# Kernel optimization log

Hardware: AMD Instinct MI355X
Metric: run time of the kernel (lower is better)

Reference implementation:

```python
import jax, jax.numpy as jnp
import numpy as np

NUM_USERS = 60000
NUM_ITEMS = 40000
NUM_NODES = NUM_USERS + NUM_ITEMS
EMBED_DIM = 64
NUM_LAYERS = 3
NUM_EDGES = 1200000
BATCH = 16384


def setup_inputs() -> dict:
    key = jax.random.key(0)
    ks = jax.random.split(key, 7)
    user_indices = jax.random.randint(ks[0], (BATCH,), 0, NUM_USERS)
    item_indices = jax.random.randint(ks[1], (BATCH,), 0, NUM_ITEMS)
    edge_rows = jax.random.randint(ks[2], (NUM_EDGES,), 0, NUM_NODES)
    edge_cols = jax.random.randint(ks[3], (NUM_EDGES,), 0, NUM_NODES)
    # normalized adjacency values are small positives ~ 1/sqrt(deg_i*deg_j)
    edge_vals = jax.random.uniform(ks[4], (NUM_EDGES,), dtype=jnp.float32) * 0.1
    # xavier_uniform for Embedding(num, dim): bound = sqrt(6/(num+dim))
    bu = float(np.sqrt(6.0 / (NUM_USERS + EMBED_DIM)))
    bi = float(np.sqrt(6.0 / (NUM_ITEMS + EMBED_DIM)))
    user_emb = jax.random.uniform(ks[5], (NUM_USERS, EMBED_DIM), jnp.float32, -bu, bu)
    item_emb = jax.random.uniform(ks[6], (NUM_ITEMS, EMBED_DIM), jnp.float32, -bi, bi)
    return {
        "user_indices": user_indices,
        "item_indices": item_indices,
        "edge_rows": edge_rows,
        "edge_cols": edge_cols,
        "edge_vals": edge_vals,
        "user_emb": user_emb,
        "item_emb": item_emb,
    }


def _spmm(edge_rows, edge_cols, edge_vals, x):
    # out[i] = sum_{e: rows[e]==i} vals[e] * x[cols[e]]  -- COO SpMM
    msgs = edge_vals[:, None] * x[edge_cols]  # [E, D]
    return jax.ops.segment_sum(msgs, edge_rows, num_segments=NUM_NODES)


def reference(user_indices, item_indices, edge_rows, edge_cols, edge_vals,
              user_emb, item_emb):
    all_embeds = jnp.concatenate([user_emb, item_emb], axis=0)  # [N, D]
    for _ in range(NUM_LAYERS):
        all_embeds = _spmm(edge_rows, edge_cols, edge_vals, all_embeds)
    all_users = all_embeds[:NUM_USERS]
    all_items = all_embeds[NUM_USERS:]
    u = all_users[user_indices]  # [B, D]
    v = all_items[item_indices]  # [B, D]
    return jnp.sum(u * v, axis=1)  # [B]
```

## Files before the change

kernel.cpp:

```cpp
#include <hip/hip_runtime.h>

#define NUM_USERS 60000
#define NUM_ITEMS 40000
#define NUM_NODES 100000
#define DIM       64
#define NUM_EDGES 1200000
#define BATCH     16384

#define BROWS 256
#define NBUCK 391
#define CAP   4096
#define EPB   4096
#define BINBLK 512
#define ZWORDS (512 + 256 + 3200)

__device__ __forceinline__ unsigned short f2bf(float f) {
    unsigned u = __float_as_uint(f);
    unsigned r = (u + 0x7FFFu + ((u >> 16) & 1u)) >> 16;
    return (unsigned short)r;
}

__global__ __launch_bounds__(256) void convert_emb(
    const float4* __restrict__ ue, const float4* __restrict__ ie,
    ushort4* __restrict__ xc, int* __restrict__ zbase)
{
    if (blockIdx.x == 0)
        for (int i = threadIdx.x; i < ZWORDS; i += 256) zbase[i] = 0;
    const int nU4 = NUM_USERS * (DIM / 4);
    const int total4 = NUM_NODES * (DIM / 4);
    int i = blockIdx.x * blockDim.x + threadIdx.x;
    int stride = gridDim.x * blockDim.x;
    for (; i < total4; i += stride) {
        float4 v = (i < nU4) ? ue[i] : ie[i - nU4];
        ushort4 s;
        s.x = f2bf(v.x); s.y = f2bf(v.y); s.z = f2bf(v.z); s.w = f2bf(v.w);
        xc[i] = s;
    }
}

__global__ __launch_bounds__(BINBLK) void bin_edges(
    const int* __restrict__ rows, const int* __restrict__ cols,
    const float* __restrict__ vals,
    const int* __restrict__ uidx, const int* __restrict__ iidx,
    int* __restrict__ gcursor, unsigned* __restrict__ flags,
    unsigned long long* __restrict__ tmp)
{
    __shared__ int cnt[NBUCK], lcur[NBUCK], gbase[NBUCK];
    int t = threadIdx.x;
    for (int i = t; i < NBUCK; i += BINBLK) { cnt[i] = 0; lcur[i] = 0; }
    int fbase = blockIdx.x * 112;
    for (int k = t; k < 112; k += BINBLK) {
        int gi = fbase + k;
        if (gi < BATCH) {
            int n = uidx[gi];
            atomicOr(&flags[n >> 5], 1u << (n & 31));
        } else if (gi < 2 * BATCH) {
            int n = NUM_USERS + iidx[gi - BATCH];
            atomicOr(&flags[n >> 5], 1u << (n & 31));
        }
    }
    __syncthreads();
    int base = blockIdx.x * EPB;
    int lim = NUM_EDGES - base; if (lim > EPB) lim = EPB;
    for (int k = t; k < lim; k += BINBLK)
        atomicAdd(&cnt[rows[base + k] >> 8], 1);
    __syncthreads();
    for (int i = t; i < NBUCK; i += BINBLK) {
        int c = cnt[i];
        gbase[i] = c ? atomicAdd(&gcursor[i], c) : 0;
    }
    __syncthreads();
    for (int k = t; k < lim; k += BINBLK) {
        int idx = base + k;
        int r = rows[idx];
        int b = r >> 8;
        int lofs = atomicAdd(&lcur[b], 1);
        unsigned long long packed =
            ((unsigned long long)(unsigned)__float_as_int(vals[idx]) << 32)
            | ((unsigned)(r & 255) << 17) | (unsigned)cols[idx];
        tmp[(size_t)b * CAP + gbase[b] + lofs] = packed;
    }
}

__global__ __launch_bounds__(256) void sort_buckets(
    const unsigned long long* __restrict__ tmp, const int* __restrict__ gcursor,
    int2* __restrict__ rse, int2* __restrict__ csr)
{
    __shared__ int lcnt[BROWS], rowcur[BROWS], sdata[BROWS];
    __shared__ int2 stage[CAP];
    int b = blockIdx.x;
    int t = threadIdx.x;
    int count = gcursor[b];
    int base  = b * CAP;
    const unsigned long long* src = tmp + (size_t)base;
    lcnt[t] = 0;
    __syncthreads();
    for (int i = t; i < count; i += 256)
        atomicAdd(&lcnt[(int)((src[i] >> 17) & 255)], 1);
    __syncthreads();
    int myc = lcnt[t];
    sdata[t] = myc;
    __syncthreads();
    #pragma unroll
    for (int off = 1; off < 256; off <<= 1) {
        int x = (t >= off) ? sdata[t - off] : 0;
        __syncthreads();
        sdata[t] += x;
        __syncthreads();
    }
    int excl = sdata[t] - myc;
    rowcur[t] = excl;
    int row = b * BROWS + t;
    if (row < NUM_NODES)
        rse[row] = make_int2(base + excl, base + excl + myc);
    __syncthreads();
    for (int i = t; i < count; i += 256) {
        unsigned long long v = src[i];
        int lr = (int)((v >> 17) & 255);
        int pos = atomicAdd(&rowcur[lr], 1);
        stage[pos] = make_int2((int)(v & 0x1FFFF), (int)(v >> 32));
    }
    __syncthreads();
    for (int i = t; i < count; i += 256)
        csr[(size_t)base + i] = stage[i];
}

__global__ __launch_bounds__(256) void compact_rows(
    const unsigned* __restrict__ flags, int* __restrict__ list,
    int* __restrict__ nrows)
{
    int i = blockIdx.x * blockDim.x + threadIdx.x;
    if (i < NUM_NODES && ((flags[i >> 5] >> (i & 31)) & 1u)) {
        int pos = atomicAdd(nrows, 1);
        list[pos] = i;
    }
}

__device__ __forceinline__ float4 bf16_row(const unsigned short* x16, int c, int q)
{
    ushort4 h = *(const ushort4*)(x16 + ((size_t)c << 6) + (q << 2));
    float4 f;
    f.x = __uint_as_float((unsigned)h.x << 16);
    f.y = __uint_as_float((unsigned)h.y << 16);
    f.z = __uint_as_float((unsigned)h.z << 16);
    f.w = __uint_as_float((unsigned)h.w << 16);
    return f;
}

__device__ __forceinline__ float4 row_accum_bf16(
    int e, int end, int q, const int2* __restrict__ csr,
    const unsigned short* __restrict__ x16)
{
    float4 acc = make_float4(0.f, 0.f, 0.f, 0.f);
    for (; e + 3 < end; e += 4) {
        int2 p0 = csr[e], p1 = csr[e + 1], p2 = csr[e + 2], p3 = csr[e + 3];
        float4 x0 = bf16_row(x16, p0.x, q);
        float4 x1 = bf16_row(x16, p1.x, q);
        float4 x2 = bf16_row(x16, p2.x, q);
        float4 x3 = bf16_row(x16, p3.x, q);
        float v0 = __int_as_float(p0.y), v1 = __int_as_float(p1.y);
        float v2 = __int_as_float(p2.y), v3 = __int_as_float(p3.y);
        acc.x = fmaf(v0, x0.x, acc.x); acc.y = fmaf(v0, x0.y, acc.y);
        acc.z = fmaf(v0, x0.z, acc.z); acc.w = fmaf(v0, x0.w, acc.w);
        acc.x = fmaf(v1, x1.x, acc.x); acc.y = fmaf(v1, x1.y, acc.y);
        acc.z = fmaf(v1, x1.z, acc.z); acc.w = fmaf(v1, x1.w, acc.w);
        acc.x = fmaf(v2, x2.x, acc.x); acc.y = fmaf(v2, x2.y, acc.y);
        acc.z = fmaf(v2, x2.z, acc.z); acc.w = fmaf(v2, x2.w, acc.w);
        acc.x = fmaf(v3, x3.x, acc.x); acc.y = fmaf(v3, x3.y, acc.y);
        acc.z = fmaf(v3, x3.z, acc.z); acc.w = fmaf(v3, x3.w, acc.w);
    }
    for (; e < end; ++e) {
        int2 p0 = csr[e];
        float4 x0 = bf16_row(x16, p0.x, q);
        float v = __int_as_float(p0.y);
        acc.x = fmaf(v, x0.x, acc.x); acc.y = fmaf(v, x0.y, acc.y);
        acc.z = fmaf(v, x0.z, acc.z); acc.w = fmaf(v, x0.w, acc.w);
    }
    return acc;
}

__global__ __launch_bounds__(256) void spmm_bb(
    const int2* __restrict__ rse, const int2* __restrict__ csr,
    const unsigned short* __restrict__ x16, unsigned short* __restrict__ y16)
{
    int tid = blockIdx.x * blockDim.x + threadIdx.x;
    int row = tid >> 4;
    if (row >= NUM_NODES) return;
    int q = tid & 15;
    int2 se = rse[row];
    float4 a = row_accum_bf16(se.x, se.y, q, csr, x16);
    ushort4 s;
    s.x = f2bf(a.x); s.y = f2bf(a.y); s.z = f2bf(a.z); s.w = f2bf(a.w);
    *(ushort4*)(y16 + ((size_t)row << 6) + (q << 2)) = s;
}

__global__ __launch_bounds__(256) void spmm_l3(
    const int* __restrict__ list, const int* __restrict__ nrowsp,
    const int2* __restrict__ rse, const int2* __restrict__ csr,
    const unsigned short* __restrict__ x16, float* __restrict__ y)
{
    int tid = blockIdx.x * blockDim.x + threadIdx.x;
    int i = tid >> 4;
    if (i >= *nrowsp) return;
    int q = tid & 15;
    int row = list[i];
    int2 se = rse[row];
    float4 acc = row_accum_bf16(se.x, se.y, q, csr, x16);
    ((float4*)y)[((size_t)row << 4) + q] = acc;
}

__global__ __launch_bounds__(256) void dot_kernel(
    const int*   __restrict__ uidx,
    const int*   __restrict__ iidx,
    const float* __restrict__ x,
    float*       __restrict__ out)
{
    int wid  = (blockIdx.x * blockDim.x + threadIdx.x) >> 6;
    int lane = threadIdx.x & 63;
    if (wid >= BATCH) return;
    int u  = uidx[wid];
    int it = iidx[wid];
    float a = x[(size_t)u * DIM + lane];
    float bb = x[((size_t)NUM_USERS + it) * DIM + lane];
    float p = a * bb;
    #pragma unroll
    for (int off = 32; off > 0; off >>= 1)
        p += __shfl_down(p, off);
    if (lane == 0) out[wid] = p;
}

extern "C" void kernel_launch(void* const* d_in, const int* in_sizes, int n_in,
                              void* d_out, int out_size, void* d_ws, size_t ws_size,
                              hipStream_t stream)
{
    const int*   user_indices = (const int*)  d_in[0];
    const int*   item_indices = (const int*)  d_in[1];
    const int*   edge_rows    = (const int*)  d_in[2];
    const int*   edge_cols    = (const int*)  d_in[3];
    const float* edge_vals    = (const float*)d_in[4];
    const float* user_emb     = (const float*)d_in[5];
    const float* item_emb     = (const float*)d_in[6];
    float*       out          = (float*)      d_out;

    const size_t nfloats = (size_t)NUM_NODES * DIM;
    char* p = (char*)d_ws;
    float* bufA = (float*)p;
    unsigned long long* tmp = (unsigned long long*)p;
    p += (size_t)NBUCK * CAP * 8;
    unsigned short* xc   = (unsigned short*)p;  p += nfloats * 2;
    unsigned short* b16B = (unsigned short*)p;  p += nfloats * 2;
    unsigned short* b16A = (unsigned short*)p;  p += nfloats * 2;
    int2*     rse     = (int2*)p;     p += 102400 * 8;
    int*      gcursor = (int*)p;      p += 512 * 4;
    int*      nrows   = (int*)p;      p += 256 * 4;
    unsigned* flags   = (unsigned*)p; p += 3200 * 4;
    int*      rowlist = (int*)p;      p += 33024 * 4;
    int2*     csr     = (int2*)p;     p += (size_t)NBUCK * CAP * 8;

    const int NB_BIN = (NUM_EDGES + EPB - 1) / EPB;

    convert_emb<<<2048, 256, 0, stream>>>(
        (const float4*)user_emb, (const float4*)item_emb, (ushort4*)xc, gcursor);
    bin_edges<<<NB_BIN, BINBLK, 0, stream>>>(
        edge_rows, edge_cols, edge_vals, user_indices, item_indices,
        gcursor, flags, tmp);
    sort_buckets<<<NBUCK, 256, 0, stream>>>(tmp, gcursor, rse, csr);
    compact_rows<<<(NUM_NODES + 255) / 256, 256, 0, stream>>>(
        flags, rowlist, nrows);

    const int NB_SPMM = (NUM_NODES * 16 + 255) / 256;
    spmm_bb<<<NB_SPMM, 256, 0, stream>>>(rse, csr, xc, b16B);
    spmm_bb<<<NB_SPMM, 256, 0, stream>>>(rse, csr, b16B, b16A);
    spmm_l3<<<(32768 * 16) / 256, 256, 0, stream>>>(
        rowlist, nrows, rse, csr, b16A, bufA);

    dot_kernel<<<(BATCH * 64) / 256, 256, 0, stream>>>(
        user_indices, item_indices, bufA, out);
}
```

Measured before the change: 138.3 us.

## Fuse prep kernels, fold row compaction into sort, widen SpMM per-thread columns

Merges the embedding conversion and edge binning into one launch, with block ranges split by role, and moves the zeroing of counters to a memset. Row-list compaction is folded into sort_buckets, which removes a separate launch. The SpMM kernels now use 8 threads per row, each handling 8 bf16 columns with 16-byte loads instead of 8-byte loads. This halves the thread count per row and gives each thread more memory-level parallelism. The aim is to cut launch overhead and improve gather efficiency, at the cost of fewer threads per row for latency hiding.

```diff
diff --git a/kernel.cpp b/kernel.cpp
--- a/kernel.cpp
+++ b/kernel.cpp
@@ -11,7 +11,9 @@
 #define NBUCK 391
 #define CAP   4096
 #define EPB   4096
-#define BINBLK 512
+#define PREPBLK 512
+#define NB_BIN 293
+#define NB_CONV 1024
 #define ZWORDS (512 + 256 + 3200)
 
 __device__ __forceinline__ unsigned short f2bf(float f) {
@@ -19,37 +21,37 @@
     unsigned r = (u + 0x7FFFu + ((u >> 16) & 1u)) >> 16;
     return (unsigned short)r;
 }
-
-__global__ __launch_bounds__(256) void convert_emb(
-    const float4* __restrict__ ue, const float4* __restrict__ ie,
-    ushort4* __restrict__ xc, int* __restrict__ zbase)
-{
-    if (blockIdx.x == 0)
-        for (int i = threadIdx.x; i < ZWORDS; i += 256) zbase[i] = 0;
-    const int nU4 = NUM_USERS * (DIM / 4);
-    const int total4 = NUM_NODES * (DIM / 4);
-    int i = blockIdx.x * blockDim.x + threadIdx.x;
-    int stride = gridDim.x * blockDim.x;
-    for (; i < total4; i += stride) {
-        float4 v = (i < nU4) ? ue[i] : ie[i - nU4];
-        ushort4 s;
-        s.x = f2bf(v.x); s.y = f2bf(v.y); s.z = f2bf(v.z); s.w = f2bf(v.w);
-        xc[i] = s;
-    }
-}
-
-__global__ __launch_bounds__(BINBLK) void bin_edges(
+__device__ __forceinline__ unsigned pack2bf(float a, float b) {
+    return (unsigned)f2bf(a) | ((unsigned)f2bf(b) << 16);
+}
+
+__global__ __launch_bounds__(PREPBLK) void prep_kernel(
     const int* __restrict__ rows, const int* __restrict__ cols,
     const float* __restrict__ vals,
     const int* __restrict__ uidx, const int* __restrict__ iidx,
+    const float4* __restrict__ ue, const float4* __restrict__ ie,
+    ushort4* __restrict__ xc,
     int* __restrict__ gcursor, unsigned* __restrict__ flags,
     unsigned long long* __restrict__ tmp)
 {
     __shared__ int cnt[NBUCK], lcur[NBUCK], gbase[NBUCK];
     int t = threadIdx.x;
-    for (int i = t; i < NBUCK; i += BINBLK) { cnt[i] = 0; lcur[i] = 0; }
+    if (blockIdx.x >= NB_BIN) {
+        const int nU4 = NUM_USERS * (DIM / 4);
+        const int total4 = NUM_NODES * (DIM / 4);
+        int i = (blockIdx.x - NB_BIN) * PREPBLK + t;
+        int stride = NB_CONV * PREPBLK;
+        for (; i < total4; i += stride) {
+            float4 v = (i < nU4) ? ue[i] : ie[i - nU4];
+            ushort4 s;
+            s.x = f2bf(v.x); s.y = f2bf(v.y); s.z = f2bf(v.z); s.w = f2bf(v.w);
+            xc[i] = s;
+        }
+        return;
+    }
+    for (int i = t; i < NBUCK; i += PREPBLK) { cnt[i] = 0; lcur[i] = 0; }
     int fbase = blockIdx.x * 112;
-    for (int k = t; k < 112; k += BINBLK) {
+    for (int k = t; k < 112; k += PREPBLK) {
         int gi = fbase + k;
         if (gi < BATCH) {
             int n = uidx[gi];
@@ -62,15 +64,15 @@
     __syncthreads();
     int base = blockIdx.x * EPB;
     int lim = NUM_EDGES - base; if (lim > EPB) lim = EPB;
-    for (int k = t; k < lim; k += BINBLK)
+    for (int k = t; k < lim; k += PREPBLK)
         atomicAdd(&cnt[rows[base + k] >> 8], 1);
     __syncthreads();
-    for (int i = t; i < NBUCK; i += BINBLK) {
+    for (int i = t; i < NBUCK; i += PREPBLK) {
         int c = cnt[i];
         gbase[i] = c ? atomicAdd(&gcursor[i], c) : 0;
     }
     __syncthreads();
-    for (int k = t; k < lim; k += BINBLK) {
+    for (int k = t; k < lim; k += PREPBLK) {
         int idx = base + k;
         int r = rows[idx];
         int b = r >> 8;
@@ -84,6 +86,8 @@
 
 __global__ __launch_bounds__(256) void sort_buckets(
     const unsigned long long* __restrict__ tmp, const int* __restrict__ gcursor,
+    const unsigned* __restrict__ flags, int* __restrict__ rowlist,
+    int* __restrict__ nrows,
     int2* __restrict__ rse, int2* __restrict__ csr)
 {
     __shared__ int lcnt[BROWS], rowcur[BROWS], sdata[BROWS];
@@ -111,8 +115,13 @@
     int excl = sdata[t] - myc;
     rowcur[t] = excl;
     int row = b * BROWS + t;
-    if (row < NUM_NODES)
+    if (row < NUM_NODES) {
         rse[row] = make_int2(base + excl, base + excl + myc);
+        if ((flags[row >> 5] >> (row & 31)) & 1u) {
+            int pos = atomicAdd(nrows, 1);
+            rowlist[pos] = row;
+        }
+    }
     __syncthreads();
     for (int i = t; i < count; i += 256) {
         unsigned long long v = src[i];
@@ -125,58 +134,47 @@
         csr[(size_t)base + i] = stage[i];
 }
 
-__global__ __launch_bounds__(256) void compact_rows(
-    const unsigned* __restrict__ flags, int* __restrict__ list,
-    int* __restrict__ nrows)
-{
-    int i = blockIdx.x * blockDim.x + threadIdx.x;
-    if (i < NUM_NODES && ((flags[i >> 5] >> (i & 31)) & 1u)) {
-        int pos = atomicAdd(nrows, 1);
-        list[pos] = i;
-    }
-}
-
-__device__ __forceinline__ float4 bf16_row(const unsigned short* x16, int c, int q)
-{
-    ushort4 h = *(const ushort4*)(x16 + ((size_t)c << 6) + (q << 2));
-    float4 f;
-    f.x = __uint_as_float((unsigned)h.x << 16);
-    f.y = __uint_as_float((unsigned)h.y << 16);
-    f.z = __uint_as_float((unsigned)h.z << 16);
-    f.w = __uint_as_float((unsigned)h.w << 16);
-    return f;
-}
-
-__device__ __forceinline__ float4 row_accum_bf16(
+__device__ __forceinline__ void fma8(
+    float acc[8], unsigned long long hx, unsigned long long hy, float v)
+{
+    unsigned h0 = (unsigned)hx, h1 = (unsigned)(hx >> 32);
+    unsigned h2 = (unsigned)hy, h3 = (unsigned)(hy >> 32);
+    acc[0] = fmaf(v, __uint_as_float(h0 << 16), acc[0]);
+    acc[1] = fmaf(v, __uint_as_float(h0 & 0xFFFF0000u), acc[1]);
+    acc[2] = fmaf(v, __uint_as_float(h1 << 16), acc[2]);
+    acc[3] = fmaf(v, __uint_as_float(h1 & 0xFFFF0000u), acc[3]);
+    acc[4] = fmaf(v, __uint_as_float(h2 << 16), acc[4]);
+    acc[5] = fmaf(v, __uint_as_float(h2 & 0xFFFF0000u), acc[5]);
+    acc[6] = fmaf(v, __uint_as_float(h3 << 16), acc[6]);
+    acc[7] = fmaf(v, __uint_as_float(h3 & 0xFFFF0000u), acc[7]);
+}
+
+__device__ __forceinline__ void row_accum8(
     int e, int end, int q, const int2* __restrict__ csr,
-    const unsigned short* __restrict__ x16)
-{
-    float4 acc = make_float4(0.f, 0.f, 0.f, 0.f);
+    const unsigned short* __restrict__ x16, float acc[8])
+{
+    typedef unsigned long long u64;
     for (; e + 3 < end; e += 4) {
         int2 p0 = csr[e], p1 = csr[e + 1], p2 = csr[e + 2], p3 = csr[e + 3];
-        float4 x0 = bf16_row(x16, p0.x, q);
-        float4 x1 = bf16_row(x16, p1.x, q);
-        float4 x2 = bf16_row(x16, p2.x, q);
-        float4 x3 = bf16_row(x16, p3.x, q);
-        float v0 = __int_as_float(p0.y), v1 = __int_as_float(p1.y);
-        float v2 = __int_as_float(p2.y), v3 = __int_as_float(p3.y);
-        acc.x = fmaf(v0, x0.x, acc.x); acc.y = fmaf(v0, x0.y, acc.y);
-        acc.z = fmaf(v0, x0.z, acc.z); acc.w = fmaf(v0, x0.w, acc.w);
-        acc.x = fmaf(v1, x1.x, acc.x); acc.y = fmaf(v1, x1.y, acc.y);
-        acc.z = fmaf(v1, x1.z, acc.z); acc.w = fmaf(v1, x1.w, acc.w);
-        acc.x = fmaf(v2, x2.x, acc.x); acc.y = fmaf(v2, x2.y, acc.y);
-        acc.z = fmaf(v2, x2.z, acc.z); acc.w = fmaf(v2, x2.w, acc.w);
-        acc.x = fmaf(v3, x3.x, acc.x); acc.y = fmaf(v3, x3.y, acc.y);
-        acc.z = fmaf(v3, x3.z, acc.z); acc.w = fmaf(v3, x3.w, acc.w);
+        const u64* s0 = (const u64*)(x16 + ((size_t)p0.x << 6) + (q << 3));
+        const u64* s1 = (const u64*)(x16 + ((size_t)p1.x << 6) + (q << 3));
+        const u64* s2 = (const u64*)(x16 + ((size_t)p2.x << 6) + (q << 3));
+        const u64* s3 = (const u64*)(x16 + ((size_t)p3.x << 6) + (q << 3));
+        u64 a0 = s0[0], b0 = s0[1];
+        u64 a1 = s1[0], b1 = s1[1];
+        u64 a2 = s2[0], b2 = s2[1];
+        u64 a3 = s3[0], b3 = s3[1];
+        fma8(acc, a0, b0, __int_as_float(p0.y));
+        fma8(acc, a1, b1, __int_as_float(p1.y));
+        fma8(acc, a2, b2, __int_as_float(p2.y));
+        fma8(acc, a3, b3, __int_as_float(p3.y));
     }
     for (; e < end; ++e) {
         int2 p0 = csr[e];
-        float4 x0 = bf16_row(x16, p0.x, q);
-        float v = __int_as_float(p0.y);
-        acc.x = fmaf(v, x0.x, acc.x); acc.y = fmaf(v, x0.y, acc.y);
-        acc.z = fmaf(v, x0.z, acc.z); acc.w = fmaf(v, x0.w, acc.w);
-    }
-    return acc;
+        const u64* s0 = (const u64*)(x16 + ((size_t)p0.x << 6) + (q << 3));
+        u64 a0 = s0[0], b0 = s0[1];
+        fma8(acc, a0, b0, __int_as_float(p0.y));
+    }
 }
 
 __global__ __launch_bounds__(256) void spmm_bb(
@@ -184,14 +182,18 @@
     const unsigned short* __restrict__ x16, unsigned short* __restrict__ y16)
 {
     int tid = blockIdx.x * blockDim.x + threadIdx.x;
-    int row = tid >> 4;
+    int row = tid >> 3;
     if (row >= NUM_NODES) return;
-    int q = tid & 15;
+    int q = tid & 7;
     int2 se = rse[row];
-    float4 a = row_accum_bf16(se.x, se.y, q, csr, x16);
-    ushort4 s;
-    s.x = f2bf(a.x); s.y = f2bf(a.y); s.z = f2bf(a.z); s.w = f2bf(a.w);
-    *(ushort4*)(y16 + ((size_t)row << 6) + (q << 2)) = s;
+    float acc[8] = {0.f, 0.f, 0.f, 0.f, 0.f, 0.f, 0.f, 0.f};
+    row_accum8(se.x, se.y, q, csr, x16, acc);
+    uint4 s;
+    s.x = pack2bf(acc[0], acc[1]);
+    s.y = pack2bf(acc[2], acc[3]);
+    s.z = pack2bf(acc[4], acc[5]);
+    s.w = pack2bf(acc[6], acc[7]);
+    *(uint4*)(y16 + ((size_t)row << 6) + (q << 3)) = s;
 }
 
 __global__ __launch_bounds__(256) void spmm_l3(
@@ -200,13 +202,16 @@
     const unsigned short* __restrict__ x16, float* __restrict__ y)
 {
     int tid = blockIdx.x * blockDim.x + threadIdx.x;
-    int i = tid >> 4;
+    int i = tid >> 3;
     if (i >= *nrowsp) return;
-    int q = tid & 15;
+    int q = tid & 7;
     int row = list[i];
     int2 se = rse[row];
-    float4 acc = row_accum_bf16(se.x, se.y, q, csr, x16);
-    ((float4*)y)[((size_t)row << 4) + q] = acc;
+    float acc[8] = {0.f, 0.f, 0.f, 0.f, 0.f, 0.f, 0.f, 0.f};
+    row_accum8(se.x, se.y, q, csr, x16, acc);
+    float4* yb = (float4*)(y + ((size_t)row << 6) + (q << 3));
+    yb[0] = make_float4(acc[0], acc[1], acc[2], acc[3]);
+    yb[1] = make_float4(acc[4], acc[5], acc[6], acc[7]);
 }
 
 __global__ __launch_bounds__(256) void dot_kernel(
@@ -257,21 +262,18 @@
     int*      rowlist = (int*)p;      p += 33024 * 4;
     int2*     csr     = (int2*)p;     p += (size_t)NBUCK * CAP * 8;
 
-    const int NB_BIN = (NUM_EDGES + EPB - 1) / EPB;
-
-    convert_emb<<<2048, 256, 0, stream>>>(
-        (const float4*)user_emb, (const float4*)item_emb, (ushort4*)xc, gcursor);
-    bin_edges<<<NB_BIN, BINBLK, 0, stream>>>(
+    hipMemsetAsync(gcursor, 0, ZWORDS * sizeof(int), stream);
+    prep_kernel<<<NB_BIN + NB_CONV, PREPBLK, 0, stream>>>(
         edge_rows, edge_cols, edge_vals, user_indices, item_indices,
+        (const float4*)user_emb, (const float4*)item_emb, (ushort4*)xc,
         gcursor, flags, tmp);
-    sort_buckets<<<NBUCK, 256, 0, stream>>>(tmp, gcursor, rse, csr);
-    compact_rows<<<(NUM_NODES + 255) / 256, 256, 0, stream>>>(
-        flags, rowlist, nrows);
-
-    const int NB_SPMM = (NUM_NODES * 16 + 255) / 256;
+    sort_buckets<<<NBUCK, 256, 0, stream>>>(
+        tmp, gcursor, flags, rowlist, nrows, rse, csr);
+
+    const int NB_SPMM = (NUM_NODES * 8 + 255) / 256;
     spmm_bb<<<NB_SPMM, 256, 0, stream>>>(rse, csr, xc, b16B);
     spmm_bb<<<NB_SPMM, 256, 0, stream>>>(rse, csr, b16B, b16A);
-    spmm_l3<<<(32768 * 16) / 256, 256, 0, stream>>>(
+    spmm_l3<<<(32768 * 8) / 256, 256, 0, stream>>>(
         rowlist, nrows, rse, csr, b16A, bufA);
 
     dot_kernel<<<(BATCH * 64) / 256, 256, 0, stream>>>(
```

After: 126.1 us. 1.1x faster.
